# Kernel optimization log

Hardware: AMD Instinct MI355X
Metric: run time of the kernel (lower is better)

## Reference

```python
import jax, jax.numpy as jnp
import numpy as np

CONV_K = 4
C_EXP = 8.0  # Griffin exponent constant
EPS = 1.1920929e-07  # torch RMSNorm default eps = finfo(float32).eps


def rmsnorm(x, w):
    return x * jax.lax.rsqrt(jnp.mean(x * x, axis=-1, keepdims=True) + EPS) * w


def gelu(x):
    return jax.nn.gelu(x, approximate=False)  # torch F.gelu default (erf)


def setup_inputs() -> dict:
    B, T, D = 16, 1024, 1024
    H = 4 * D  # GatedMLP hidden
    key = jax.random.key(0)
    ks = jax.random.split(key, 16)
    s = 0.02
    return {
        "x_seq": jax.random.normal(ks[0], (B, T, D), jnp.float32),
        "h0": jnp.zeros((B, D), jnp.float32),
        "conv_buf": jax.random.normal(ks[1], (B, CONV_K - 1, D), jnp.float32),
        "norm1_w": jnp.ones((D,), jnp.float32),
        "W1": jax.random.normal(ks[2], (D, D), jnp.float32) * s,
        "conv_w": jax.random.normal(ks[3], (D, CONV_K), jnp.float32) * s,
        "conv_b": jnp.zeros((D,), jnp.float32),
        "Wa": jax.random.normal(ks[4], (D, D), jnp.float32) * s,
        "ba": jnp.zeros((D,), jnp.float32),
        "Wx": jax.random.normal(ks[5], (D, D), jnp.float32) * s,
        "bx": jnp.zeros((D,), jnp.float32),
        "log_lambda": jnp.linspace(0.0, 4.0, D).astype(jnp.float32),
        "W2": jax.random.normal(ks[6], (D, D), jnp.float32) * s,
        "Wout": jax.random.normal(ks[7], (D, D), jnp.float32) * s,
        "norm2_w": jnp.ones((D,), jnp.float32),
        "Wg": jax.random.normal(ks[8], (H, D), jnp.float32) * s,
        "Wu": jax.random.normal(ks[9], (H, D), jnp.float32) * s,
        "Wo": jax.random.normal(ks[10], (D, H), jnp.float32) * s,
    }


def _block(x_seq, h0, conv_buf, norm1_w, W1, conv_w, conv_b, Wa, ba, Wx, bx,
           log_lambda, W2, Wout, norm2_w, Wg, Wu, Wo):
    B, T, D = x_seq.shape
    normed = rmsnorm(x_seq, norm1_w)
    b1 = normed @ W1.T                                   # (B,T,D)
    padded = jnp.concatenate([conv_buf, b1], axis=1)     # (B,T+3,D)
    # depthwise causal conv (cross-correlation, matching torch Conv1d)
    b1_conv = conv_b
    for k in range(CONV_K):
        b1_conv = b1_conv + padded[:, k:k + T, :] * conv_w[:, k]
    new_conv_buf = padded[:, -(CONV_K - 1):, :]

    # RG-LRU: precompute gates, scan only the diagonal linear recurrence
    r = jax.nn.sigmoid(b1_conv @ Wa.T + ba)
    i = jax.nn.sigmoid(b1_conv @ Wx.T + bx)
    a = jnp.exp((C_EXP * r) * jax.nn.log_sigmoid(log_lambda))  # sigmoid(L)**(c*r)
    gate = jnp.sqrt(jnp.clip((1.0 - a) * (1.0 + a), 1e-06))
    u = gate * (i * b1_conv)

    def step(h, au):
        a_t, u_t = au
        h = a_t * h + u_t
        return h, h

    new_h, outs = jax.lax.scan(step, h0,
                               (jnp.swapaxes(a, 0, 1), jnp.swapaxes(u, 0, 1)))
    b1_out = jnp.swapaxes(outs, 0, 1)                    # (B,T,D)

    b2 = gelu(normed @ W2.T)
    recurrent_out = (b1_out * b2) @ Wout.T
    x1 = x_seq + recurrent_out

    n2 = rmsnorm(x1, norm2_w)
    mlp = (gelu(n2 @ Wg.T) * (n2 @ Wu.T)) @ Wo.T         # GeGLU gated MLP
    x2 = x1 + mlp
    return x2, new_h, new_conv_buf


def reference(x_seq, h0, conv_buf, norm1_w, W1, conv_w, conv_b, Wa, ba, Wx, bx,
              log_lambda, W2, Wout, norm2_w, Wg, Wu, Wo):
    return _block(x_seq, h0, conv_buf, norm1_w, W1, conv_w, conv_b, Wa, ba,
                  Wx, bx, log_lambda, W2, Wout, norm2_w, Wg, Wu, Wo)
```

## Files before the change

### kernel.cpp

```cpp
#include <hip/hip_runtime.h>
#include <hip/hip_bf16.h>
#include <cstdint>

using bf16 = __hip_bfloat16;
typedef __attribute__((ext_vector_type(8))) short bf16x8;
typedef __attribute__((ext_vector_type(4))) float f32x4;

#define NB 16
#define NT_ 1024
#define ND 1024
#define NH 4096
#define NM (NB * NT_)

enum { EPI_BF16 = 0, EPI_OM, EPI_U, EPI_GELU, EPI_GELU_MUL, EPI_X1, EPI_X2 };

__device__ __forceinline__ float sigm(float x) { return 1.0f / (1.0f + expf(-x)); }
__device__ __forceinline__ float gelu_f(float x) { return 0.5f * x * (1.0f + erff(x * 0.7071067811865476f)); }
__device__ __forceinline__ float b2f(bf16 h) { return __bfloat162float(h); }
__device__ __forceinline__ bf16  f2b(float x) { return __float2bfloat16(x); }

__device__ __forceinline__ void gl_lds16(const bf16* g, void* l) {
  __builtin_amdgcn_global_load_lds((const __attribute__((address_space(1))) void*)g,
                                   (__attribute__((address_space(3))) void*)l, 16, 0, 0);
}

template <int EPI>
__global__ __launch_bounds__(256)
void gemm_nt(const bf16* __restrict__ A, const bf16* __restrict__ Bw,
             int M, int N, int K,
             const float* __restrict__ biasf, const float* __restrict__ vecf,
             const bf16* __restrict__ auxb, const bf16* __restrict__ auxb2,
             const float* __restrict__ auxf,
             float* __restrict__ outf, bf16* __restrict__ outb)
{
  __shared__ __align__(16) bf16 As[128 * 32];
  __shared__ __align__(16) bf16 Bs[128 * 32];
  const int tid  = threadIdx.x;
  const int wave = tid >> 6, lane = tid & 63;
  const int lr = lane & 15, lq = lane >> 4;
  const int m0 = blockIdx.y * 128, n0 = blockIdx.x * 128;
  const int wm = (wave & 1) * 64, wn = (wave >> 1) * 64;

  f32x4 acc[4][4];
#pragma unroll
  for (int i = 0; i < 4; ++i)
#pragma unroll
    for (int j = 0; j < 4; ++j)
#pragma unroll
      for (int r = 0; r < 4; ++r) acc[i][j][r] = 0.0f;

  const bf16* Ab = A  + (long)m0 * K;
  const bf16* Bb = Bw + (long)n0 * K;
  const int row0 = tid >> 2;
  const int kp0  = (tid & 3) << 3;

  for (int k0 = 0; k0 < K; k0 += 32) {
    __syncthreads();
    gl_lds16(Ab + (long)row0 * K + k0 + kp0,        ((char*)As) + tid * 16);
    gl_lds16(Bb + (long)row0 * K + k0 + kp0,        ((char*)Bs) + tid * 16);
    gl_lds16(Ab + (long)(row0 + 64) * K + k0 + kp0, ((char*)As) + (tid + 256) * 16);
    gl_lds16(Bb + (long)(row0 + 64) * K + k0 + kp0, ((char*)Bs) + (tid + 256) * 16);
    __syncthreads();

    bf16x8 af[4], bfr[4];
#pragma unroll
    for (int i = 0; i < 4; ++i)
      af[i] = *reinterpret_cast<const bf16x8*>(&As[(wm + i * 16 + lr) * 32 + lq * 8]);
#pragma unroll
    for (int j = 0; j < 4; ++j)
      bfr[j] = *reinterpret_cast<const bf16x8*>(&Bs[(wn + j * 16 + lr) * 32 + lq * 8]);
#pragma unroll
    for (int i = 0; i < 4; ++i)
#pragma unroll
      for (int j = 0; j < 4; ++j)
        acc[i][j] = __builtin_amdgcn_mfma_f32_16x16x32_bf16(af[i], bfr[j], acc[i][j], 0, 0, 0);
  }

#pragma unroll
  for (int i = 0; i < 4; ++i) {
#pragma unroll
    for (int j = 0; j < 4; ++j) {
#pragma unroll
      for (int r = 0; r < 4; ++r) {
        const int row = m0 + wm + i * 16 + lq * 4 + r;
        const int col = n0 + wn + j * 16 + lr;
        const long idx = (long)row * N + col;
        float v = acc[i][j][r];
        if constexpr (EPI == EPI_BF16) {
          outb[idx] = f2b(v);
        } else if constexpr (EPI == EPI_OM) {
          float rr = sigm(v + biasf[col]);
          float ls = -log1pf(expf(-vecf[col]));
          outb[idx] = f2b(-expm1f(8.0f * rr * ls));
        } else if constexpr (EPI == EPI_U) {
          float ii = sigm(v + biasf[col]);
          float om = b2f(auxb2[idx]);
          float g  = sqrtf(fmaxf(om * (2.0f - om), 1e-6f));
          outb[idx] = f2b(g * ii * b2f(auxb[idx]));
        } else if constexpr (EPI == EPI_GELU) {
          outb[idx] = f2b(gelu_f(v));
        } else if constexpr (EPI == EPI_GELU_MUL) {
          float u2 = b2f(outb[idx]);
          outb[idx] = f2b(gelu_f(v) * u2);
        } else if constexpr (EPI == EPI_X1) {
          outb[idx] = f2b(v + auxf[idx]);
        } else if constexpr (EPI == EPI_X2) {
          outf[idx] = v + b2f(auxb[idx]);
        }
      }
    }
  }
}

__global__ __launch_bounds__(256)
void cast4_kernel(const float* __restrict__ in, bf16* __restrict__ out, long n4) {
  long i = (long)blockIdx.x * 256 + threadIdx.x;
  if (i < n4) {
    float4 v = reinterpret_cast<const float4*>(in)[i];
    union { bf16 h[4]; ushort4 u; } pk;
    pk.h[0] = f2b(v.x); pk.h[1] = f2b(v.y); pk.h[2] = f2b(v.z); pk.h[3] = f2b(v.w);
    reinterpret_cast<ushort4*>(out)[i] = pk.u;
  }
}

template <typename TIN>
__global__ __launch_bounds__(256)
void rmsnorm_kernel(const TIN* __restrict__ x, const float* __restrict__ w,
                    bf16* __restrict__ out) {
  const int row = blockIdx.x;
  const int t = threadIdx.x;
  float4 v;
  if constexpr (sizeof(TIN) == 4) {
    v = reinterpret_cast<const float4*>(x + (long)row * ND)[t];
  } else {
    union { ushort4 u; bf16 h[4]; } xv;
    xv.u = reinterpret_cast<const ushort4*>(x + (long)row * ND)[t];
    v = make_float4(b2f(xv.h[0]), b2f(xv.h[1]), b2f(xv.h[2]), b2f(xv.h[3]));
  }
  float ss = v.x * v.x + v.y * v.y + v.z * v.z + v.w * v.w;
#pragma unroll
  for (int off = 32; off > 0; off >>= 1) ss += __shfl_down(ss, off, 64);
  __shared__ float red[4];
  if ((t & 63) == 0) red[t >> 6] = ss;
  __syncthreads();
  float tot = red[0] + red[1] + red[2] + red[3];
  float scale = rsqrtf(tot * (1.0f / ND) + 1.1920929e-07f);
  float4 wv = reinterpret_cast<const float4*>(w)[t];
  union { bf16 h[4]; ushort4 u; } pk;
  pk.h[0] = f2b(v.x * scale * wv.x);
  pk.h[1] = f2b(v.y * scale * wv.y);
  pk.h[2] = f2b(v.z * scale * wv.z);
  pk.h[3] = f2b(v.w * scale * wv.w);
  reinterpret_cast<ushort4*>(out + (long)row * ND)[t] = pk.u;
}

__global__ __launch_bounds__(256)
void conv_kernel(const bf16* __restrict__ b1, const float* __restrict__ conv_buf,
                 const float* __restrict__ conv_w, const float* __restrict__ conv_b,
                 bf16* __restrict__ out_b1c, float* __restrict__ out_newbuf) {
  const long gid = (long)blockIdx.x * 256 + threadIdx.x;
  const int d = (int)(gid & (ND - 1));
  const long bt = gid >> 10;
  const int t = (int)(bt & (NT_ - 1));
  const int b = (int)(bt >> 10);
  float acc = conv_b[d];
#pragma unroll
  for (int k = 0; k < 4; ++k) {
    const int p = t + k;
    float src = (p < 3) ? conv_buf[((long)b * 3 + p) * ND + d]
                        : b2f(b1[((long)b * NT_ + (p - 3)) * ND + d]);
    acc = fmaf(conv_w[d * 4 + k], src, acc);
  }
  out_b1c[gid] = f2b(acc);
  if (t >= NT_ - 3)
    out_newbuf[((long)b * 3 + (t - (NT_ - 3))) * ND + d] = b2f(b1[gid]);
}

__global__ __launch_bounds__(256)
void scan_kernel(const bf16* __restrict__ om, const bf16* __restrict__ u,
                 const bf16* __restrict__ b2, const float* __restrict__ h0,
                 bf16* __restrict__ prod, float* __restrict__ newh) {
  const int gid = blockIdx.x * 256 + threadIdx.x;
  const int d = gid & (ND - 1);
  const int b = gid >> 10;
  float h = h0[gid];
  const long base = (long)b * NT_ * ND + d;
#pragma unroll 8
  for (int t = 0; t < NT_; ++t) {
    const long idx = base + (long)t * ND;
    h = fmaf(-b2f(om[idx]), h, h) + b2f(u[idx]);
    prod[idx] = f2b(h * b2f(b2[idx]));
  }
  newh[gid] = h;
}

extern "C" void kernel_launch(void* const* d_in, const int* in_sizes, int n_in,
                              void* d_out, int out_size, void* d_ws, size_t ws_size,
                              hipStream_t stream) {
  const float* x_seq    = (const float*)d_in[0];
  const float* h0       = (const float*)d_in[1];
  const float* conv_buf = (const float*)d_in[2];
  const float* norm1_w  = (const float*)d_in[3];
  const float* W1       = (const float*)d_in[4];
  const float* conv_w   = (const float*)d_in[5];
  const float* conv_b   = (const float*)d_in[6];
  const float* Wa       = (const float*)d_in[7];
  const float* ba       = (const float*)d_in[8];
  const float* Wx       = (const float*)d_in[9];
  const float* bx       = (const float*)d_in[10];
  const float* loglam   = (const float*)d_in[11];
  const float* W2       = (const float*)d_in[12];
  const float* Wout     = (const float*)d_in[13];
  const float* norm2_w  = (const float*)d_in[14];
  const float* Wg       = (const float*)d_in[15];
  const float* Wu       = (const float*)d_in[16];
  const float* Wo       = (const float*)d_in[17];

  char* ws = (char*)d_ws;
  bf16* normed = (bf16*)(ws);
  bf16* b1buf  = (bf16*)(ws + (32L  << 20));
  bf16* b1cbuf = (bf16*)(ws + (64L  << 20));
  bf16* Woutb  = (bf16*)(ws + (64L  << 20));
  bf16* ombuf  = (bf16*)(ws + (96L  << 20));
  bf16* ubuf   = (bf16*)(ws + (128L << 20));
  bf16* x1buf  = (bf16*)(ws + (160L << 20));
  bf16* b2buf  = x1buf;
  bf16* bigbuf = (bf16*)(ws + (32L  << 20));
  bf16* W1b    = (bf16*)(ws + (192L << 20));
  bf16* Wab    = (bf16*)(ws + (194L << 20));
  bf16* Wxb    = (bf16*)(ws + (196L << 20));
  bf16* W2b    = (bf16*)(ws + (198L << 20));
  bf16* Wgb    = (bf16*)(ws + (200L << 20));
  bf16* Wub    = (bf16*)(ws + (208L << 20));
  bf16* Wob    = (bf16*)(ws + (216L << 20));

  float* out_x2 = (float*)d_out;
  float* out_h  = out_x2 + (long)NM * ND;
  float* out_cb = out_h + NB * ND;

  const dim3 blk(256);
  const dim3 gD(ND / 128, NM / 128);
  const dim3 gH(NH / 128, NM / 128);

  cast4_kernel<<<dim3(1024), blk, 0, stream>>>(W1, W1b, 262144);
  cast4_kernel<<<dim3(1024), blk, 0, stream>>>(Wa, Wab, 262144);
  cast4_kernel<<<dim3(1024), blk, 0, stream>>>(Wx, Wxb, 262144);
  cast4_kernel<<<dim3(1024), blk, 0, stream>>>(W2, W2b, 262144);
  cast4_kernel<<<dim3(4096), blk, 0, stream>>>(Wg, Wgb, 1048576);
  cast4_kernel<<<dim3(4096), blk, 0, stream>>>(Wu, Wub, 1048576);
  cast4_kernel<<<dim3(4096), blk, 0, stream>>>(Wo, Wob, 1048576);

  rmsnorm_kernel<float><<<dim3(NM), blk, 0, stream>>>(x_seq, norm1_w, normed);
  gemm_nt<EPI_BF16><<<gD, blk, 0, stream>>>(normed, W1b, NM, ND, ND,
      nullptr, nullptr, nullptr, nullptr, nullptr, nullptr, b1buf);
  conv_kernel<<<dim3((NM * ND) / 256), blk, 0, stream>>>(b1buf, conv_buf, conv_w, conv_b,
      b1cbuf, out_cb);
  gemm_nt<EPI_OM><<<gD, blk, 0, stream>>>(b1cbuf, Wab, NM, ND, ND,
      ba, loglam, nullptr, nullptr, nullptr, nullptr, ombuf);
  gemm_nt<EPI_U><<<gD, blk, 0, stream>>>(b1cbuf, Wxb, NM, ND, ND,
      bx, nullptr, b1cbuf, ombuf, nullptr, nullptr, ubuf);
  gemm_nt<EPI_GELU><<<gD, blk, 0, stream>>>(normed, W2b, NM, ND, ND,
      nullptr, nullptr, nullptr, nullptr, nullptr, nullptr, b2buf);
  scan_kernel<<<dim3(NB * ND / 256), blk, 0, stream>>>(ombuf, ubuf, b2buf, h0, b1buf, out_h);
  cast4_kernel<<<dim3(1024), blk, 0, stream>>>(Wout, Woutb, 262144);
  gemm_nt<EPI_X1><<<gD, blk, 0, stream>>>(b1buf, Woutb, NM, ND, ND,
      nullptr, nullptr, nullptr, nullptr, x_seq, nullptr, x1buf);
  rmsnorm_kernel<bf16><<<dim3(NM), blk, 0, stream>>>(x1buf, norm2_w, normed);
  gemm_nt<EPI_BF16><<<gH, blk, 0, stream>>>(normed, Wub, NM, NH, ND,
      nullptr, nullptr, nullptr, nullptr, nullptr, nullptr, bigbuf);
  gemm_nt<EPI_GELU_MUL><<<gH, blk, 0, stream>>>(normed, Wgb, NM, NH, ND,
      nullptr, nullptr, nullptr, nullptr, nullptr, nullptr, bigbuf);
  gemm_nt<EPI_X2><<<gD, blk, 0, stream>>>(bigbuf, Wob, NM, ND, NH,
      nullptr, nullptr, x1buf, nullptr, nullptr, out_x2, nullptr);
}
```

Measured before the change: 1.405 ms.

## Fuse paired GEMMs sharing an A operand into dual-B kernels; shrink scan blocks

Adds a gemm2_nt kernel that loads one A tile and two weight tiles per k-step and keeps two accumulator sets. It fuses W1/W2, Wa/Wx and Wg/Wu into three launches instead of six, so the shared activation is read once and the gate/up intermediate no longer round-trips through memory. The scan kernel now uses 64-thread blocks, which spreads the 16K sequential threads over more CUs. The cost is double the accumulator registers (128 floats of accumulators per thread) and more LDS per block, which may lower occupancy or cause register spills.

```diff
diff --git a/kernel.cpp b/kernel.cpp
--- a/kernel.cpp
+++ b/kernel.cpp
@@ -12,7 +12,8 @@
 #define NH 4096
 #define NM (NB * NT_)
 
-enum { EPI_BF16 = 0, EPI_OM, EPI_U, EPI_GELU, EPI_GELU_MUL, EPI_X1, EPI_X2 };
+enum { EPI_X1 = 0, EPI_X2 };
+enum { P_B1B2 = 0, P_OMU, P_MLP };
 
 __device__ __forceinline__ float sigm(float x) { return 1.0f / (1.0f + expf(-x)); }
 __device__ __forceinline__ float gelu_f(float x) { return 0.5f * x * (1.0f + erff(x * 0.7071067811865476f)); }
@@ -28,9 +29,7 @@
 __global__ __launch_bounds__(256)
 void gemm_nt(const bf16* __restrict__ A, const bf16* __restrict__ Bw,
              int M, int N, int K,
-             const float* __restrict__ biasf, const float* __restrict__ vecf,
-             const bf16* __restrict__ auxb, const bf16* __restrict__ auxb2,
-             const float* __restrict__ auxf,
+             const bf16* __restrict__ auxb, const float* __restrict__ auxf,
              float* __restrict__ outf, bf16* __restrict__ outb)
 {
   __shared__ __align__(16) bf16 As[128 * 32];
@@ -80,32 +79,109 @@
   for (int i = 0; i < 4; ++i) {
 #pragma unroll
     for (int j = 0; j < 4; ++j) {
+      const int col = n0 + wn + j * 16 + lr;
 #pragma unroll
       for (int r = 0; r < 4; ++r) {
         const int row = m0 + wm + i * 16 + lq * 4 + r;
-        const int col = n0 + wn + j * 16 + lr;
         const long idx = (long)row * N + col;
         float v = acc[i][j][r];
-        if constexpr (EPI == EPI_BF16) {
-          outb[idx] = f2b(v);
-        } else if constexpr (EPI == EPI_OM) {
-          float rr = sigm(v + biasf[col]);
-          float ls = -log1pf(expf(-vecf[col]));
-          outb[idx] = f2b(-expm1f(8.0f * rr * ls));
-        } else if constexpr (EPI == EPI_U) {
-          float ii = sigm(v + biasf[col]);
-          float om = b2f(auxb2[idx]);
+        if constexpr (EPI == EPI_X1) {
+          outb[idx] = f2b(v + auxf[idx]);
+        } else {
+          outf[idx] = v + b2f(auxb[idx]);
+        }
+      }
+    }
+  }
+}
+
+template <int EPI>
+__global__ __launch_bounds__(256)
+void gemm2_nt(const bf16* __restrict__ A, const bf16* __restrict__ B1w,
+              const bf16* __restrict__ B2w, int M, int N, int K,
+              const float* __restrict__ bias1, const float* __restrict__ bias2,
+              const float* __restrict__ vecf, const bf16* __restrict__ auxb,
+              bf16* __restrict__ out1, bf16* __restrict__ out2)
+{
+  __shared__ __align__(16) bf16 As [128 * 32];
+  __shared__ __align__(16) bf16 B1s[128 * 32];
+  __shared__ __align__(16) bf16 B2s[128 * 32];
+  const int tid  = threadIdx.x;
+  const int wave = tid >> 6, lane = tid & 63;
+  const int lr = lane & 15, lq = lane >> 4;
+  const int m0 = blockIdx.y * 128, n0 = blockIdx.x * 128;
+  const int wm = (wave & 1) * 64, wn = (wave >> 1) * 64;
+
+  f32x4 acc1[4][4], acc2[4][4];
+#pragma unroll
+  for (int i = 0; i < 4; ++i)
+#pragma unroll
+    for (int j = 0; j < 4; ++j)
+#pragma unroll
+      for (int r = 0; r < 4; ++r) { acc1[i][j][r] = 0.0f; acc2[i][j][r] = 0.0f; }
+
+  const bf16* Ab  = A   + (long)m0 * K;
+  const bf16* B1b = B1w + (long)n0 * K;
+  const bf16* B2b = B2w + (long)n0 * K;
+  const int row0 = tid >> 2;
+  const int kp0  = (tid & 3) << 3;
+
+  for (int k0 = 0; k0 < K; k0 += 32) {
+    __syncthreads();
+    gl_lds16(Ab  + (long)row0 * K + k0 + kp0,        ((char*)As)  + tid * 16);
+    gl_lds16(B1b + (long)row0 * K + k0 + kp0,        ((char*)B1s) + tid * 16);
+    gl_lds16(B2b + (long)row0 * K + k0 + kp0,        ((char*)B2s) + tid * 16);
+    gl_lds16(Ab  + (long)(row0 + 64) * K + k0 + kp0, ((char*)As)  + (tid + 256) * 16);
+    gl_lds16(B1b + (long)(row0 + 64) * K + k0 + kp0, ((char*)B1s) + (tid + 256) * 16);
+    gl_lds16(B2b + (long)(row0 + 64) * K + k0 + kp0, ((char*)B2s) + (tid + 256) * 16);
+    __syncthreads();
+
+    bf16x8 af[4], bf1[4], bf2[4];
+#pragma unroll
+    for (int i = 0; i < 4; ++i)
+      af[i] = *reinterpret_cast<const bf16x8*>(&As[(wm + i * 16 + lr) * 32 + lq * 8]);
+#pragma unroll
+    for (int j = 0; j < 4; ++j) {
+      bf1[j] = *reinterpret_cast<const bf16x8*>(&B1s[(wn + j * 16 + lr) * 32 + lq * 8]);
+      bf2[j] = *reinterpret_cast<const bf16x8*>(&B2s[(wn + j * 16 + lr) * 32 + lq * 8]);
+    }
+#pragma unroll
+    for (int i = 0; i < 4; ++i)
+#pragma unroll
+      for (int j = 0; j < 4; ++j) {
+        acc1[i][j] = __builtin_amdgcn_mfma_f32_16x16x32_bf16(af[i], bf1[j], acc1[i][j], 0, 0, 0);
+        acc2[i][j] = __builtin_amdgcn_mfma_f32_16x16x32_bf16(af[i], bf2[j], acc2[i][j], 0, 0, 0);
+      }
+  }
+
+#pragma unroll
+  for (int i = 0; i < 4; ++i) {
+#pragma unroll
+    for (int j = 0; j < 4; ++j) {
+      const int col = n0 + wn + j * 16 + lr;
+      float bb1 = 0.f, bb2 = 0.f, ls = 0.f;
+      if constexpr (EPI == P_OMU) {
+        bb1 = bias1[col];
+        bb2 = bias2[col];
+        ls  = -log1pf(expf(-vecf[col]));
+      }
+#pragma unroll
+      for (int r = 0; r < 4; ++r) {
+        const int row = m0 + wm + i * 16 + lq * 4 + r;
+        const long idx = (long)row * N + col;
+        float v1 = acc1[i][j][r], v2 = acc2[i][j][r];
+        if constexpr (EPI == P_B1B2) {
+          out1[idx] = f2b(v1);
+          out2[idx] = f2b(gelu_f(v2));
+        } else if constexpr (EPI == P_OMU) {
+          float rr = sigm(v1 + bb1);
+          float om = -expm1f(8.0f * rr * ls);
+          float ii = sigm(v2 + bb2);
           float g  = sqrtf(fmaxf(om * (2.0f - om), 1e-6f));
-          outb[idx] = f2b(g * ii * b2f(auxb[idx]));
-        } else if constexpr (EPI == EPI_GELU) {
-          outb[idx] = f2b(gelu_f(v));
-        } else if constexpr (EPI == EPI_GELU_MUL) {
-          float u2 = b2f(outb[idx]);
-          outb[idx] = f2b(gelu_f(v) * u2);
-        } else if constexpr (EPI == EPI_X1) {
-          outb[idx] = f2b(v + auxf[idx]);
-        } else if constexpr (EPI == EPI_X2) {
-          outf[idx] = v + b2f(auxb[idx]);
+          out1[idx] = f2b(om);
+          out2[idx] = f2b(g * ii * b2f(auxb[idx]));
+        } else {
+          out2[idx] = f2b(gelu_f(v1) * v2);
         }
       }
     }
@@ -176,11 +252,11 @@
     out_newbuf[((long)b * 3 + (t - (NT_ - 3))) * ND + d] = b2f(b1[gid]);
 }
 
-__global__ __launch_bounds__(256)
+__global__ __launch_bounds__(64)
 void scan_kernel(const bf16* __restrict__ om, const bf16* __restrict__ u,
                  const bf16* __restrict__ b2, const float* __restrict__ h0,
                  bf16* __restrict__ prod, float* __restrict__ newh) {
-  const int gid = blockIdx.x * 256 + threadIdx.x;
+  const int gid = blockIdx.x * 64 + threadIdx.x;
   const int d = gid & (ND - 1);
   const int b = gid >> 10;
   float h = h0[gid];
@@ -251,25 +327,19 @@
   cast4_kernel<<<dim3(4096), blk, 0, stream>>>(Wo, Wob, 1048576);
 
   rmsnorm_kernel<float><<<dim3(NM), blk, 0, stream>>>(x_seq, norm1_w, normed);
-  gemm_nt<EPI_BF16><<<gD, blk, 0, stream>>>(normed, W1b, NM, ND, ND,
-      nullptr, nullptr, nullptr, nullptr, nullptr, nullptr, b1buf);
+  gemm2_nt<P_B1B2><<<gD, blk, 0, stream>>>(normed, W1b, W2b, NM, ND, ND,
+      nullptr, nullptr, nullptr, nullptr, b1buf, b2buf);
   conv_kernel<<<dim3((NM * ND) / 256), blk, 0, stream>>>(b1buf, conv_buf, conv_w, conv_b,
       b1cbuf, out_cb);
-  gemm_nt<EPI_OM><<<gD, blk, 0, stream>>>(b1cbuf, Wab, NM, ND, ND,
-      ba, loglam, nullptr, nullptr, nullptr, nullptr, ombuf);
-  gemm_nt<EPI_U><<<gD, blk, 0, stream>>>(b1cbuf, Wxb, NM, ND, ND,
-      bx, nullptr, b1cbuf, ombuf, nullptr, nullptr, ubuf);
-  gemm_nt<EPI_GELU><<<gD, blk, 0, stream>>>(normed, W2b, NM, ND, ND,
-      nullptr, nullptr, nullptr, nullptr, nullptr, nullptr, b2buf);
-  scan_kernel<<<dim3(NB * ND / 256), blk, 0, stream>>>(ombuf, ubuf, b2buf, h0, b1buf, out_h);
+  gemm2_nt<P_OMU><<<gD, blk, 0, stream>>>(b1cbuf, Wab, Wxb, NM, ND, ND,
+      ba, bx, loglam, b1cbuf, ombuf, ubuf);
+  scan_kernel<<<dim3(NB * ND / 64), dim3(64), 0, stream>>>(ombuf, ubuf, b2buf, h0, b1buf, out_h);
   cast4_kernel<<<dim3(1024), blk, 0, stream>>>(Wout, Woutb, 262144);
   gemm_nt<EPI_X1><<<gD, blk, 0, stream>>>(b1buf, Woutb, NM, ND, ND,
-      nullptr, nullptr, nullptr, nullptr, x_seq, nullptr, x1buf);
+      nullptr, x_seq, nullptr, x1buf);
   rmsnorm_kernel<bf16><<<dim3(NM), blk, 0, stream>>>(x1buf, norm2_w, normed);
-  gemm_nt<EPI_BF16><<<gH, blk, 0, stream>>>(normed, Wub, NM, NH, ND,
-      nullptr, nullptr, nullptr, nullptr, nullptr, nullptr, bigbuf);
-  gemm_nt<EPI_GELU_MUL><<<gH, blk, 0, stream>>>(normed, Wgb, NM, NH, ND,
-      nullptr, nullptr, nullptr, nullptr, nullptr, nullptr, bigbuf);
+  gemm2_nt<P_MLP><<<gH, blk, 0, stream>>>(normed, Wgb, Wub, NM, NH, ND,
+      nullptr, nullptr, nullptr, nullptr, nullptr, bigbuf);
   gemm_nt<EPI_X2><<<gD, blk, 0, stream>>>(bigbuf, Wob, NM, ND, NH,
-      nullptr, nullptr, x1buf, nullptr, nullptr, out_x2, nullptr);
-}
+      x1buf, nullptr, out_x2, nullptr);
+}
```

After: 1.783 ms. 1.27x slower.
